# Performance work log

Hardware: AMD Instinct MI355X
Metric: run time of the kernel (lower is better)

## Reference

```python
import jax, jax.numpy as jnp
import numpy as np

N_NODES = 100000
N_EDGES = 3200000
EPS = 1e-5
NEG_SLOPE = 0.1


def _glorot(key, fan_in, fan_out):
    lim = np.sqrt(6.0 / (fan_in + fan_out))
    return jax.random.uniform(key, (fan_in, fan_out), jnp.float32, -lim, lim)


def setup_inputs() -> dict:
    key = jax.random.key(0)
    ks = jax.random.split(key, 16)
    x = jax.random.normal(ks[0], (N_NODES, 3), jnp.float32)
    edge_index = jax.random.randint(ks[1], (2, N_EDGES), 0, N_NODES, jnp.int32)
    dims = [(3, 64), (64, 64), (64, 256), (256, 256), (256, 512), (512, 1)]
    inp = {"x": x, "edge_index": edge_index}
    for i, (fi, fo) in enumerate(dims):
        inp[f"W{i+1}"] = _glorot(ks[2 + i], fi, fo)
        inp[f"b{i+1}"] = jnp.zeros((fo,), jnp.float32)
    for i, fo in enumerate([64, 64, 256, 256, 512]):
        inp[f"g{i+1}"] = jnp.ones((fo,), jnp.float32)
        inp[f"bt{i+1}"] = jnp.zeros((fo,), jnp.float32)
    return inp


def _gcn_conv(h, W, b, src, dst, dis):
    # transform first (cheaper when out_dim <= in_dim is not guaranteed, but
    # avoids gathering raw features twice); then edge-normalized scatter-add.
    hw = h @ W                                   # [N, Fo]
    norm = dis[src] * dis[dst]                   # [E]
    agg = jax.ops.segment_sum(hw[src] * norm[:, None], dst, num_segments=N_NODES)
    agg = agg + (dis * dis)[:, None] * hw        # self-loop term (norm = dis_i^2)
    return agg + b


def _bn(h, g, bt):
    mu = jnp.mean(h, axis=0)
    var = jnp.mean((h - mu) ** 2, axis=0)        # biased var, as torch BN
    return (h - mu) * jax.lax.rsqrt(var + EPS) * g + bt


def _lrelu(h):
    return jnp.where(h > 0, h, NEG_SLOPE * h)


def reference(x, edge_index, W1, b1, W2, b2, W3, b3, W4, b4, W5, b5, W6, b6,
              g1, bt1, g2, bt2, g3, bt3, g4, bt4, g5, bt5):
    src, dst = edge_index[0], edge_index[1]
    # degree includes the added self-loop (+1), symmetric normalization
    deg = jax.ops.segment_sum(jnp.ones((N_EDGES,), x.dtype), dst,
                              num_segments=N_NODES) + 1.0
    dis = jax.lax.rsqrt(deg)

    h = x
    Ws = [W1, W2, W3, W4, W5]
    bs = [b1, b2, b3, b4, b5]
    gs = [g1, g2, g3, g4, g5]
    bts = [bt1, bt2, bt3, bt4, bt5]
    for W, b, g, bt in zip(Ws, bs, gs, bts):
        h = _gcn_conv(h, W, b, src, dst, dis)
        h = _lrelu(_bn(h, g, bt))
    h = _gcn_conv(h, W6, b6, src, dst, dis)
    return jax.nn.sigmoid(h)
```

## Files before the change

kernel.cpp:

```cpp
#include <hip/hip_runtime.h>
#include <math.h>

typedef unsigned short u16;
typedef unsigned int u32;
typedef __attribute__((ext_vector_type(8))) short bf16x8;
typedef __attribute__((ext_vector_type(4))) float f32x4;
typedef __attribute__((ext_vector_type(2))) float f32x2;

constexpr float EPS_BN = 1e-5f;
constexpr float NEG = 0.1f;
constexpr int LDP = 800;

static inline int cdiv(int a, int b) { return (a + b - 1) / b; }


__device__ __forceinline__ float b2f_lo(u32 v) { return __uint_as_float(v << 16); }
__device__ __forceinline__ float b2f_hi(u32 v) { return __uint_as_float(v & 0xFFFF0000u); }
__device__ __forceinline__ float b2f(u16 v) { return __uint_as_float(((u32)v) << 16); }
__device__ __forceinline__ u16 f2b(float f) {
  u32 u = __float_as_uint(f);
  u32 r = u + 0x7FFFu + ((u >> 16) & 1u);
  return (u16)(r >> 16);
}
__device__ __forceinline__ u32 pack2(float a, float b) {
  return (u32)f2b(a) | ((u32)f2b(b) << 16);
}
__device__ __forceinline__ void unpack8(uint4 v, float* o) {
  o[0] = b2f_lo(v.x); o[1] = b2f_hi(v.x);
  o[2] = b2f_lo(v.y); o[3] = b2f_hi(v.y);
  o[4] = b2f_lo(v.z); o[5] = b2f_hi(v.z);
  o[6] = b2f_lo(v.w); o[7] = b2f_hi(v.w);
}

__device__ __forceinline__ void gload16(const void* g, void* l) {
  __builtin_amdgcn_global_load_lds(
      (const __attribute__((address_space(1))) u32*)g,
      (__attribute__((address_space(3))) u32*)l, 16, 0, 0);
}

__device__ __forceinline__ void bn8_acc(uint4 v, const f32x2* sc2, const f32x2* sh2,
                                        float d, f32x2* acc) {
  const f32x2 dd = {d, d};
  const f32x2 c01 = {NEG, NEG};
  const u32* w = &v.x;
#pragma unroll
  for (int p = 0; p < 4; ++p) {
    f32x2 z = {b2f_lo(w[p]), b2f_hi(w[p])};
    f32x2 t = z * sc2[p] + sh2[p];
    f32x2 q = __builtin_elementwise_max(t, t * c01);
    acc[p] = dd * q + acc[p];
  }
}


__global__ void k_zero_i32(int* p, int n) {
  int i = blockIdx.x * blockDim.x + threadIdx.x;
  if (i < n) p[i] = 0;
}

__global__ __launch_bounds__(256) void k_bcount(const int* __restrict__ dst,
                                                int* __restrict__ bucketCnt, int E) {
  __shared__ int hist[256];
  int tid = threadIdx.x;
  hist[tid] = 0;
  __syncthreads();
  int e0 = blockIdx.x * 4096;
#pragma unroll
  for (int i = 0; i < 16; ++i) {
    int e = e0 + i * 256 + tid;
    if (e < E) atomicAdd(&hist[dst[e] >> 9], 1);
  }
  __syncthreads();
  int h = hist[tid];
  if (h > 0) atomicAdd(&bucketCnt[tid], h);
}

__global__ void k_bscan(const int* __restrict__ bucketCnt, int* __restrict__ bucketOff,
                        int* __restrict__ bucketCur, int NB, int E) {
  __shared__ int s[256];
  int tid = threadIdx.x;
  int v = (tid < NB) ? bucketCnt[tid] : 0;
  s[tid] = v;
  __syncthreads();
  for (int off = 1; off < 256; off <<= 1) {
    int t = (tid >= off) ? s[tid - off] : 0;
    __syncthreads();
    s[tid] += t;
    __syncthreads();
  }
  if (tid < NB) bucketOff[tid] = s[tid] - v;
  if (tid == NB) bucketOff[NB] = E;
  if (tid < NB) bucketCur[tid] = 0;
}

__global__ __launch_bounds__(256) void k_bucket(const int* __restrict__ src,
                                                const int* __restrict__ dst,
                                                const int* __restrict__ bucketOff,
                                                int* __restrict__ bucketCur,
                                                u32* __restrict__ ebuf, int E) {
  __shared__ int hist[256];
  __shared__ int base[256];
  __shared__ int lcur[256];
  int tid = threadIdx.x;
  hist[tid] = 0; lcur[tid] = 0;
  __syncthreads();
  int e0 = blockIdx.x * 4096;
  int ss[16], dd[16];
#pragma unroll
  for (int i = 0; i < 16; ++i) {
    int e = e0 + i * 256 + tid;
    if (e < E) {
      ss[i] = src[e]; dd[i] = dst[e];
      atomicAdd(&hist[dd[i] >> 9], 1);
    } else dd[i] = -1;
  }
  __syncthreads();
  int h = hist[tid];
  if (h > 0) base[tid] = bucketOff[tid] + atomicAdd(&bucketCur[tid], h);
  __syncthreads();
#pragma unroll
  for (int i = 0; i < 16; ++i) {
    if (dd[i] >= 0) {
      int bk = dd[i] >> 9;
      int p = atomicAdd(&lcur[bk], 1);
      ebuf[base[bk] + p] = ((u32)ss[i] << 9) | ((u32)dd[i] & 511u);
    }
  }
}

__global__ __launch_bounds__(256) void k_csr(const u32* __restrict__ ebuf,
                                             const int* __restrict__ bucketOff,
                                             int* __restrict__ rowoff,
                                             int* __restrict__ col,
                                             float* __restrict__ dis,
                                             int N, int E, int NB) {
  __shared__ int hist[512];
  __shared__ int loff[512];
  __shared__ int scan_s[256];
  int b = blockIdx.x;
  int tid = threadIdx.x;
  int ebase = bucketOff[b], eend = bucketOff[b + 1];
  int ecnt = eend - ebase;
  hist[tid] = 0; hist[tid + 256] = 0;
  __syncthreads();
  for (int i = tid; i < ecnt; i += 256)
    atomicAdd(&hist[ebuf[ebase + i] & 511u], 1);
  __syncthreads();
  int h0 = hist[2 * tid], h1 = hist[2 * tid + 1];
  int ts = h0 + h1;
  scan_s[tid] = ts;
  __syncthreads();
  for (int off = 1; off < 256; off <<= 1) {
    int t = (tid >= off) ? scan_s[tid - off] : 0;
    __syncthreads();
    scan_s[tid] += t;
    __syncthreads();
  }
  int excl = scan_s[tid] - ts;
  loff[2 * tid] = excl;
  loff[2 * tid + 1] = excl + h0;
  __syncthreads();
  int gbase = b * 512;
  for (int i = tid; i < 512; i += 256) {
    int node = gbase + i;
    if (node < N) {
      rowoff[node] = ebase + loff[i];
      dis[node] = rsqrtf((float)hist[i] + 1.0f);
    }
  }
  if (b == NB - 1 && tid == 0) rowoff[N] = E;
  __syncthreads();
  for (int i = tid; i < ecnt; i += 256) {
    u32 ed = ebuf[ebase + i];
    int p = atomicAdd(&loff[ed & 511u], 1);
    col[ebase + p] = (int)(ed >> 9);
  }
}


__global__ void k_xd(const float* __restrict__ x, const float* __restrict__ dis,
                     float4* __restrict__ xd, int n) {
  int i = blockIdx.x * blockDim.x + threadIdx.x;
  if (i >= n) return;
  float d = dis[i];
  xd[i] = make_float4(d * x[i * 3 + 0], d * x[i * 3 + 1], d * x[i * 3 + 2], 0.f);
}

__global__ void k_l1(const float4* __restrict__ xd, const int* __restrict__ rowoff,
                     const int* __restrict__ col, const float* __restrict__ dis,
                     const float* __restrict__ W, const float* __restrict__ b,
                     u16* __restrict__ z, int n) {
  int wid = (blockIdx.x * blockDim.x + threadIdx.x) >> 6;
  int lane = threadIdx.x & 63;
  if (wid >= n) return;
  float a0 = 0.f, a1 = 0.f, a2 = 0.f;
  int beg = rowoff[wid], end = rowoff[wid + 1];
  for (int e = beg + lane; e < end; e += 64) {
    float4 v = xd[col[e]];
    a0 += v.x; a1 += v.y; a2 += v.z;
  }
#pragma unroll
  for (int off = 32; off; off >>= 1) {
    a0 += __shfl_xor(a0, off); a1 += __shfl_xor(a1, off); a2 += __shfl_xor(a2, off);
  }
  float di = dis[wid];
  float4 sv = xd[wid];
  a0 = di * (a0 + sv.x);
  a1 = di * (a1 + sv.y);
  a2 = di * (a2 + sv.z);
  float zv = a0 * W[lane] + a1 * W[64 + lane] + a2 * W[128 + lane] + b[lane];
  z[(size_t)wid * 64 + lane] = f2b(zv);
}


__global__ void k_agg64(const u16* __restrict__ z, const int* __restrict__ rowoff,
                        const int* __restrict__ col, const float* __restrict__ dis,
                        const float* __restrict__ scaleF, const float* __restrict__ shiftF,
                        u16* __restrict__ a, int n) {
  int wid = (blockIdx.x * blockDim.x + threadIdx.x) >> 6;
  int lane = threadIdx.x & 63;
  if (wid >= n) return;
  int sub = lane >> 3, c = lane & 7;
  const uint4* z4 = (const uint4*)z;
  f32x2 sc2[4], sh2[4];
#pragma unroll
  for (int p = 0; p < 4; ++p) {
    sc2[p] = *(const f32x2*)&scaleF[c * 8 + p * 2];
    sh2[p] = *(const f32x2*)&shiftF[c * 8 + p * 2];
  }
  f32x2 acc[4] = {{0.f, 0.f}, {0.f, 0.f}, {0.f, 0.f}, {0.f, 0.f}};
  int beg = rowoff[wid], end = rowoff[wid + 1];
  int e = beg + sub;
  int j1 = (e < end) ? col[e] : -1;
  int j2 = (e + 8 < end) ? col[e + 8] : -1;
  float d1 = (j1 >= 0) ? dis[j1] : 0.f;
  float d2 = (j2 >= 0) ? dis[j2] : 0.f;
  while (j1 >= 0) {
    int en = e + 16;
    int nj1 = -1, nj2 = -1;
    if (j2 >= 0) {
      if (en < end) nj1 = col[en];
      if (en + 8 < end) nj2 = col[en + 8];
    }
    float nd1 = (nj1 >= 0) ? dis[nj1] : 0.f;
    float nd2 = (nj2 >= 0) ? dis[nj2] : 0.f;
    bn8_acc(z4[(size_t)j1 * 8 + c], sc2, sh2, d1, acc);
    if (j2 >= 0) bn8_acc(z4[(size_t)j2 * 8 + c], sc2, sh2, d2, acc);
    e = en; j1 = nj1; j2 = nj2; d1 = nd1; d2 = nd2;
  }
  float* af = (float*)acc;
#pragma unroll
  for (int k = 0; k < 8; ++k) {
    af[k] += __shfl_xor(af[k], 8);
    af[k] += __shfl_xor(af[k], 16);
    af[k] += __shfl_xor(af[k], 32);
  }
  if (sub == 0) {
    float dw = dis[wid];
    bn8_acc(z4[(size_t)wid * 8 + c], sc2, sh2, dw, acc);
    uint4 r;
    r.x = pack2(dw * af[0], dw * af[1]);
    r.y = pack2(dw * af[2], dw * af[3]);
    r.z = pack2(dw * af[4], dw * af[5]);
    r.w = pack2(dw * af[6], dw * af[7]);
    ((uint4*)a)[(size_t)wid * 8 + c] = r;
  }
}

__global__ void k_agg256(const u16* __restrict__ z, const int* __restrict__ rowoff,
                         const int* __restrict__ col, const float* __restrict__ dis,
                         const float* __restrict__ scaleF, const float* __restrict__ shiftF,
                         u16* __restrict__ a, int n) {
  int wid = (blockIdx.x * blockDim.x + threadIdx.x) >> 6;
  int lane = threadIdx.x & 63;
  if (wid >= n) return;
  int sub = lane >> 5, c = lane & 31;
  const uint4* z4 = (const uint4*)z;
  f32x2 sc2[4], sh2[4];
#pragma unroll
  for (int p = 0; p < 4; ++p) {
    sc2[p] = *(const f32x2*)&scaleF[c * 8 + p * 2];
    sh2[p] = *(const f32x2*)&shiftF[c * 8 + p * 2];
  }
  f32x2 acc[4] = {{0.f, 0.f}, {0.f, 0.f}, {0.f, 0.f}, {0.f, 0.f}};
  int beg = rowoff[wid], end = rowoff[wid + 1];
  int e = beg + sub;
  int j1 = (e < end) ? col[e] : -1;
  int j2 = (e + 2 < end) ? col[e + 2] : -1;
  float d1 = (j1 >= 0) ? dis[j1] : 0.f;
  float d2 = (j2 >= 0) ? dis[j2] : 0.f;
  while (j1 >= 0) {
    int en = e + 4;
    int nj1 = -1, nj2 = -1;
    if (j2 >= 0) {
      if (en < end) nj1 = col[en];
      if (en + 2 < end) nj2 = col[en + 2];
    }
    float nd1 = (nj1 >= 0) ? dis[nj1] : 0.f;
    float nd2 = (nj2 >= 0) ? dis[nj2] : 0.f;
    bn8_acc(z4[(size_t)j1 * 32 + c], sc2, sh2, d1, acc);
    if (j2 >= 0) bn8_acc(z4[(size_t)j2 * 32 + c], sc2, sh2, d2, acc);
    e = en; j1 = nj1; j2 = nj2; d1 = nd1; d2 = nd2;
  }
  float* af = (float*)acc;
#pragma unroll
  for (int k = 0; k < 8; ++k) af[k] += __shfl_xor(af[k], 32);
  if (sub == 0) {
    float dw = dis[wid];
    bn8_acc(z4[(size_t)wid * 32 + c], sc2, sh2, dw, acc);
    uint4 r;
    r.x = pack2(dw * af[0], dw * af[1]);
    r.y = pack2(dw * af[2], dw * af[3]);
    r.z = pack2(dw * af[4], dw * af[5]);
    r.w = pack2(dw * af[6], dw * af[7]);
    ((uint4*)a)[(size_t)wid * 32 + c] = r;
  }
}


__global__ void k_wt_all(const float* __restrict__ W2, const float* __restrict__ W3,
                         const float* __restrict__ W4, const float* __restrict__ W5,
                         u16* __restrict__ WT) {
  int i = blockIdx.x * blockDim.x + threadIdx.x;
  const float* W; int K, Fo, base;
  if (i < 4096)        { W = W2; K = 64;  Fo = 64;  base = 0; }
  else if (i < 20480)  { W = W3; K = 64;  Fo = 256; base = 4096; }
  else if (i < 86016)  { W = W4; K = 256; Fo = 256; base = 20480; }
  else if (i < 217088) { W = W5; K = 256; Fo = 512; base = 86016; }
  else return;
  int idx = i - base;
  int f = idx / K, k = idx - f * K;
  WT[i] = f2b(W[(size_t)k * Fo + f]);
}


__global__ __launch_bounds__(256) void k_gemm(const u16* __restrict__ A,
                                              const u16* __restrict__ WT,
                                              const float* __restrict__ bias,
                                              u16* __restrict__ C,
                                              float* __restrict__ psum,
                                              float* __restrict__ psq,
                                              int n, int K, int Fo, int nby) {
  __shared__ u16 As[128 * 64];
  __shared__ u16 Bs[128 * 64];
  int tid = threadIdx.x;
  int nwg = gridDim.x;
  int bid = blockIdx.x;
  int q = nwg >> 3, rr = nwg & 7;
  int xcd = bid & 7, pos = bid >> 3;
  int wgid = (xcd < rr ? xcd * (q + 1) : rr * (q + 1) + (xcd - rr) * q) + pos;
  int bx = wgid / nby, by = wgid - bx * nby;
  int bm0 = bx * 128, bn0 = by * 128;
  int lane = tid & 63, wv = tid >> 6;
  int wm = wv >> 1, wn = wv & 1;
  int fr = lane & 15, fg = lane >> 4;
  int srow = lane >> 3;
  int cb = (lane & 7) ^ srow;
  f32x4 acc[4][4];
#pragma unroll
  for (int i = 0; i < 4; ++i)
#pragma unroll
    for (int j = 0; j < 4; ++j) acc[i][j] = (f32x4)0.0f;

  for (int kt = 0; kt < K; kt += 64) {
#pragma unroll
    for (int i = 0; i < 4; ++i) {
      int rb = 8 * (4 * wv + i);
      const u16* ga = &A[(size_t)(bm0 + rb + srow) * K + kt + cb * 8];
      gload16(ga, &As[rb * 64 + lane * 8]);
      const u16* gb = &WT[(size_t)(bn0 + rb + srow) * K + kt + cb * 8];
      gload16(gb, &Bs[rb * 64 + lane * 8]);
    }
    __syncthreads();
#pragma unroll
    for (int ks = 0; ks < 2; ++ks) {
      int k0 = ks * 32 + fg * 8;
      bf16x8 af[4], bf[4];
#pragma unroll
      for (int mi = 0; mi < 4; ++mi) {
        int row = wm * 64 + mi * 16 + fr;
        int byt = (row * 128 + k0 * 2) ^ ((row & 7) << 4);
        af[mi] = *(const bf16x8*)((const char*)As + byt);
      }
#pragma unroll
      for (int ni = 0; ni < 4; ++ni) {
        int row = wn * 64 + ni * 16 + fr;
        int byt = (row * 128 + k0 * 2) ^ ((row & 7) << 4);
        bf[ni] = *(const bf16x8*)((const char*)Bs + byt);
      }
#pragma unroll
      for (int mi = 0; mi < 4; ++mi)
#pragma unroll
        for (int ni = 0; ni < 4; ++ni)
          acc[mi][ni] = __builtin_amdgcn_mfma_f32_16x16x32_bf16(af[mi], bf[ni], acc[mi][ni], 0, 0, 0);
    }
    __syncthreads();
  }
  float* s2 = (float*)&As[0];
#pragma unroll
  for (int ni = 0; ni < 4; ++ni) {
    int gc = bn0 + wn * 64 + ni * 16 + fr;
    float ps = 0.f, pq = 0.f;
    if (gc < Fo) {
      float bv = bias[gc];
#pragma unroll
      for (int mi = 0; mi < 4; ++mi) {
#pragma unroll
        for (int rg = 0; rg < 4; ++rg) {
          int gr = bm0 + wm * 64 + mi * 16 + fg * 4 + rg;
          if (gr < n) {
            float v = acc[mi][ni][rg] + bv;
            C[(size_t)gr * Fo + gc] = f2b(v);
            ps += v; pq += v * v;
          }
        }
      }
    }
    ps += __shfl_xor(ps, 16); ps += __shfl_xor(ps, 32);
    pq += __shfl_xor(pq, 16); pq += __shfl_xor(pq, 32);
    if (fg == 0 && gc < Fo) {
      int cl = wn * 64 + ni * 16 + fr;
      s2[wm * 128 + cl] = ps;
      s2[256 + wm * 128 + cl] = pq;
    }
  }
  __syncthreads();
  if (tid < 128) {
    int gc = bn0 + tid;
    if (gc < Fo) {
      psum[(size_t)gc * LDP + bx] = s2[tid] + s2[128 + tid];
      psq[(size_t)gc * LDP + bx] = s2[256 + tid] + s2[384 + tid];
    }
  }
}


__global__ void k_colred(const u16* __restrict__ z, int Fo, int n, int rowsPerChunk,
                         float* __restrict__ psum, float* __restrict__ psq) {
  int fl = threadIdx.x & 63;
  int rg = threadIdx.x >> 6;
  int f = blockIdx.y * 64 + fl;
  int r0 = blockIdx.x * rowsPerChunk;
  int r1 = min(n, r0 + rowsPerChunk);
  float s = 0.f, sq = 0.f;
  for (int r = r0 + rg; r < r1; r += 4) {
    float v = b2f(z[(size_t)r * Fo + f]);
    s += v;
    sq += v * v;
  }
  __shared__ float ls[4][64], lq[4][64];
  ls[rg][fl] = s; lq[rg][fl] = sq;
  __syncthreads();
  if (rg == 0) {
    psum[(size_t)f * LDP + blockIdx.x] = ls[0][fl] + ls[1][fl] + ls[2][fl] + ls[3][fl];
    psq[(size_t)f * LDP + blockIdx.x] = lq[0][fl] + lq[1][fl] + lq[2][fl] + lq[3][fl];
  }
}

__global__ void k_bnparams(const float* __restrict__ psum, const float* __restrict__ psq,
                           int Fo, int nChunks, int n,
                           const float* __restrict__ g, const float* __restrict__ bt,
                           float* __restrict__ scaleF, float* __restrict__ shiftF) {
  int f = blockIdx.x * 4 + (threadIdx.x >> 6);
  int lane = threadIdx.x & 63;
  if (f >= Fo) return;
  float s = 0.f, sq = 0.f;
  const float* ps = &psum[(size_t)f * LDP];
  const float* pq = &psq[(size_t)f * LDP];
  for (int c = lane; c < nChunks; c += 64) { s += ps[c]; sq += pq[c]; }
#pragma unroll
  for (int off = 32; off; off >>= 1) {
    s += __shfl_xor(s, off);
    sq += __shfl_xor(sq, off);
  }
  if (lane == 0) {
    float inv = 1.0f / (float)n;
    float mu = s * inv;
    float var = sq * inv - mu * mu;
    float rs = rsqrtf(var + EPS_BN) * g[f];
    scaleF[f] = rs;
    shiftF[f] = bt[f] - mu * rs;
  }
}


__global__ void k_dot512(const u16* __restrict__ z, const float* __restrict__ scaleF,
                         const float* __restrict__ shiftF, const float* __restrict__ w6,
                         const float* __restrict__ dis, float* __restrict__ v, int n) {
  __shared__ float ws[512], scs[512], shs[512];
  int tid = threadIdx.x;
  for (int i = tid; i < 512; i += 256) { ws[i] = w6[i]; scs[i] = scaleF[i]; shs[i] = shiftF[i]; }
  __syncthreads();
  int lane = tid % 64, wv = tid / 64;
  int node = blockIdx.x * 4 + wv;
  if (node >= n) return;
  uint4 vz = *(const uint4*)&z[(size_t)node * 512 + lane * 8];
  float f[8];
  unpack8(vz, f);
  int f0 = lane * 8;
  float s = 0.f;
#pragma unroll
  for (int k = 0; k < 8; ++k) {
    float a = f[k] * scs[f0 + k] + shs[f0 + k];
    a = (a > 0.f) ? a : NEG * a;
    s += a * ws[f0 + k];
  }
#pragma unroll
  for (int off = 32; off > 0; off >>= 1) s += __shfl_down(s, off);
  if (lane == 0) v[node] = dis[node] * s;
}

__global__ void k_final(const float* __restrict__ v, const int* __restrict__ rowoff,
                        const int* __restrict__ col, const float* __restrict__ dis,
                        const float* __restrict__ b6, float* __restrict__ out, int n) {
  int wid = (blockIdx.x * blockDim.x + threadIdx.x) >> 6;
  int lane = threadIdx.x & 63;
  if (wid >= n) return;
  float acc = 0.f;
  int beg = rowoff[wid], end = rowoff[wid + 1];
  for (int e = beg + lane; e < end; e += 64) acc += v[col[e]];
#pragma unroll
  for (int off = 32; off; off >>= 1) acc += __shfl_xor(acc, off);
  if (lane == 0) {
    float zz = dis[wid] * (acc + v[wid]) + b6[0];
    out[wid] = 1.0f / (1.0f + expf(-zz));
  }
}


extern "C" void kernel_launch(void* const* d_in, const int* in_sizes, int n_in,
                              void* d_out, int out_size, void* d_ws, size_t ws_size,
                              hipStream_t stream) {
  const float* x = (const float*)d_in[0];
  const int* ei = (const int*)d_in[1];
  const int N = in_sizes[0] / 3;
  const int E = in_sizes[1] / 2;
  const int* srcIdx = ei;
  const int* dstIdx = ei + E;

  const float* W[6]; const float* b[6];
  for (int i = 0; i < 6; ++i) { W[i] = (const float*)d_in[2 + 2 * i]; b[i] = (const float*)d_in[3 + 2 * i]; }
  const float* g[5]; const float* bt[5];
  for (int i = 0; i < 5; ++i) { g[i] = (const float*)d_in[14 + 2 * i]; bt[i] = (const float*)d_in[15 + 2 * i]; }

  char* wsB = (char*)d_ws;
  size_t off = 0;
  auto alloc = [&](size_t bytes) -> void* {
    void* p = wsB + off;
    off = (off + bytes + 255) & ~(size_t)255;
    return p;
  };

  const int NB = cdiv(N, 512);
  int* rowoff = (int*)alloc((size_t)(N + 1) * 4);
  int* col = (int*)alloc((size_t)E * 4);
  float* dis = (float*)alloc((size_t)N * 4);
  float* vbuf = (float*)alloc((size_t)N * 4);
  float* scaleF = (float*)alloc(512 * 4);
  float* shiftF = (float*)alloc(512 * 4);
  float4* xd = (float4*)alloc((size_t)N * 16);
  u16* WTb = (u16*)alloc((size_t)217088 * 2);
  int* bucketCnt = (int*)alloc(256 * 4);
  int* bucketOff = (int*)alloc(257 * 4);
  int* bucketCur = (int*)alloc(256 * 4);
  const int nbx = cdiv(N, 128);
  float* psum = (float*)alloc((size_t)512 * LDP * 4);
  float* psq = (float*)alloc((size_t)512 * LDP * 4);
  u16* Zb = (u16*)alloc((size_t)N * 512 * 2);
  u16* Ab = (u16*)alloc((size_t)(N + 128) * 256 * 2);
  u32* ebuf = (u32*)Ab;

  const int wtOff[5] = {0, 0, 4096, 20480, 86016};
  k_wt_all<<<cdiv(217088, 256), 256, 0, stream>>>(W[1], W[2], W[3], W[4], WTb);

  const int EB = cdiv(E, 4096);
  k_zero_i32<<<1, 256, 0, stream>>>(bucketCnt, 256);
  k_bcount<<<EB, 256, 0, stream>>>(dstIdx, bucketCnt, E);
  k_bscan<<<1, 256, 0, stream>>>(bucketCnt, bucketOff, bucketCur, NB, E);
  k_bucket<<<EB, 256, 0, stream>>>(srcIdx, dstIdx, bucketOff, bucketCur, ebuf, E);
  k_csr<<<NB, 256, 0, stream>>>(ebuf, bucketOff, rowoff, col, dis, N, E, NB);

  auto gemm = [&](const u16* Ain, int layer, int K, int Fo, u16* Cout) {
    int nby = cdiv(Fo, 128);
    k_gemm<<<nbx * nby, 256, 0, stream>>>(Ain, WTb + wtOff[layer], b[layer], Cout,
                                          psum, psq, N, K, Fo, nby);
    k_bnparams<<<cdiv(Fo, 4), 256, 0, stream>>>(psum, psq, Fo, nbx, N,
                                                g[layer], bt[layer], scaleF, shiftF);
  };

  const int waveGrid = cdiv(N * 64, 256);

  k_xd<<<cdiv(N, 256), 256, 0, stream>>>(x, dis, xd, N);
  k_l1<<<waveGrid, 256, 0, stream>>>(xd, rowoff, col, dis, W[0], b[0], Zb, N);
  {
    const int rowsPerChunk = 2048;
    const int nChunks = cdiv(N, rowsPerChunk);
    dim3 grid(nChunks, 1);
    k_colred<<<grid, 256, 0, stream>>>(Zb, 64, N, rowsPerChunk, psum, psq);
    k_bnparams<<<cdiv(64, 4), 256, 0, stream>>>(psum, psq, 64, nChunks, N, g[0], bt[0], scaleF, shiftF);
  }

  k_agg64<<<waveGrid, 256, 0, stream>>>(Zb, rowoff, col, dis, scaleF, shiftF, Ab, N);
  gemm(Ab, 1, 64, 64, Zb);

  k_agg64<<<waveGrid, 256, 0, stream>>>(Zb, rowoff, col, dis, scaleF, shiftF, Ab, N);
  gemm(Ab, 2, 64, 256, Zb);

  k_agg256<<<waveGrid, 256, 0, stream>>>(Zb, rowoff, col, dis, scaleF, shiftF, Ab, N);
  gemm(Ab, 3, 256, 256, Zb);

  k_agg256<<<waveGrid, 256, 0, stream>>>(Zb, rowoff, col, dis, scaleF, shiftF, Ab, N);
  gemm(Ab, 4, 256, 512, Zb);

  k_dot512<<<cdiv(N, 4), 256, 0, stream>>>(Zb, scaleF, shiftF, W[5], dis, vbuf, N);
  k_final<<<waveGrid, 256, 0, stream>>>(vbuf, rowoff, col, dis, b[5], (float*)d_out, N);
}
```

Measured before the change: 1.154 ms.

## Split aggregation feature columns across XCD halves and fold xd into CSR build

```diff
diff --git a/kernel.cpp b/kernel.cpp
--- a/kernel.cpp
+++ b/kernel.cpp
@@ -130,9 +130,11 @@
 
 __global__ __launch_bounds__(256) void k_csr(const u32* __restrict__ ebuf,
                                              const int* __restrict__ bucketOff,
+                                             const float* __restrict__ x,
                                              int* __restrict__ rowoff,
                                              int* __restrict__ col,
                                              float* __restrict__ dis,
+                                             float4* __restrict__ xd,
                                              int N, int E, int NB) {
   __shared__ int hist[512];
   __shared__ int loff[512];
@@ -165,7 +167,10 @@
     int node = gbase + i;
     if (node < N) {
       rowoff[node] = ebase + loff[i];
-      dis[node] = rsqrtf((float)hist[i] + 1.0f);
+      float d = rsqrtf((float)hist[i] + 1.0f);
+      dis[node] = d;
+      xd[node] = make_float4(d * x[node * 3 + 0], d * x[node * 3 + 1],
+                             d * x[node * 3 + 2], 0.f);
     }
   }
   if (b == NB - 1 && tid == 0) rowoff[N] = E;
@@ -177,14 +182,6 @@
   }
 }
 
-
-__global__ void k_xd(const float* __restrict__ x, const float* __restrict__ dis,
-                     float4* __restrict__ xd, int n) {
-  int i = blockIdx.x * blockDim.x + threadIdx.x;
-  if (i >= n) return;
-  float d = dis[i];
-  xd[i] = make_float4(d * x[i * 3 + 0], d * x[i * 3 + 1], d * x[i * 3 + 2], 0.f);
-}
 
 __global__ void k_l1(const float4* __restrict__ xd, const int* __restrict__ rowoff,
                      const int* __restrict__ col, const float* __restrict__ dis,
@@ -217,53 +214,60 @@
                         const int* __restrict__ col, const float* __restrict__ dis,
                         const float* __restrict__ scaleF, const float* __restrict__ shiftF,
                         u16* __restrict__ a, int n) {
-  int wid = (blockIdx.x * blockDim.x + threadIdx.x) >> 6;
+  int bid = blockIdx.x;
+  int xcd = bid & 7;
+  int half = xcd >> 2;
+  int slot = ((bid >> 3) << 2) + (xcd & 3);
+  int node = (slot << 2) + (threadIdx.x >> 6);
+  if (node >= n) return;
   int lane = threadIdx.x & 63;
-  if (wid >= n) return;
-  int sub = lane >> 3, c = lane & 7;
+  int sub = lane >> 2, c = lane & 3;
   const uint4* z4 = (const uint4*)z;
   f32x2 sc2[4], sh2[4];
+  int f0 = half * 32 + c * 8;
 #pragma unroll
   for (int p = 0; p < 4; ++p) {
-    sc2[p] = *(const f32x2*)&scaleF[c * 8 + p * 2];
-    sh2[p] = *(const f32x2*)&shiftF[c * 8 + p * 2];
-  }
+    sc2[p] = *(const f32x2*)&scaleF[f0 + p * 2];
+    sh2[p] = *(const f32x2*)&shiftF[f0 + p * 2];
+  }
+  int rb = half * 4 + c;
   f32x2 acc[4] = {{0.f, 0.f}, {0.f, 0.f}, {0.f, 0.f}, {0.f, 0.f}};
-  int beg = rowoff[wid], end = rowoff[wid + 1];
+  int beg = rowoff[node], end = rowoff[node + 1];
   int e = beg + sub;
   int j1 = (e < end) ? col[e] : -1;
-  int j2 = (e + 8 < end) ? col[e + 8] : -1;
+  int j2 = (e + 16 < end) ? col[e + 16] : -1;
   float d1 = (j1 >= 0) ? dis[j1] : 0.f;
   float d2 = (j2 >= 0) ? dis[j2] : 0.f;
   while (j1 >= 0) {
-    int en = e + 16;
+    int en = e + 32;
     int nj1 = -1, nj2 = -1;
     if (j2 >= 0) {
       if (en < end) nj1 = col[en];
-      if (en + 8 < end) nj2 = col[en + 8];
+      if (en + 16 < end) nj2 = col[en + 16];
     }
     float nd1 = (nj1 >= 0) ? dis[nj1] : 0.f;
     float nd2 = (nj2 >= 0) ? dis[nj2] : 0.f;
-    bn8_acc(z4[(size_t)j1 * 8 + c], sc2, sh2, d1, acc);
-    if (j2 >= 0) bn8_acc(z4[(size_t)j2 * 8 + c], sc2, sh2, d2, acc);
+    bn8_acc(z4[(size_t)j1 * 8 + rb], sc2, sh2, d1, acc);
+    if (j2 >= 0) bn8_acc(z4[(size_t)j2 * 8 + rb], sc2, sh2, d2, acc);
     e = en; j1 = nj1; j2 = nj2; d1 = nd1; d2 = nd2;
   }
   float* af = (float*)acc;
 #pragma unroll
   for (int k = 0; k < 8; ++k) {
+    af[k] += __shfl_xor(af[k], 4);
     af[k] += __shfl_xor(af[k], 8);
     af[k] += __shfl_xor(af[k], 16);
     af[k] += __shfl_xor(af[k], 32);
   }
   if (sub == 0) {
-    float dw = dis[wid];
-    bn8_acc(z4[(size_t)wid * 8 + c], sc2, sh2, dw, acc);
+    float dw = dis[node];
+    bn8_acc(z4[(size_t)node * 8 + rb], sc2, sh2, dw, acc);
     uint4 r;
     r.x = pack2(dw * af[0], dw * af[1]);
     r.y = pack2(dw * af[2], dw * af[3]);
     r.z = pack2(dw * af[4], dw * af[5]);
     r.w = pack2(dw * af[6], dw * af[7]);
-    ((uint4*)a)[(size_t)wid * 8 + c] = r;
+    ((uint4*)a)[(size_t)node * 8 + rb] = r;
   }
 }
 
@@ -271,49 +275,58 @@
                          const int* __restrict__ col, const float* __restrict__ dis,
                          const float* __restrict__ scaleF, const float* __restrict__ shiftF,
                          u16* __restrict__ a, int n) {
-  int wid = (blockIdx.x * blockDim.x + threadIdx.x) >> 6;
+  int bid = blockIdx.x;
+  int xcd = bid & 7;
+  int half = xcd >> 2;
+  int slot = ((bid >> 3) << 2) + (xcd & 3);
+  int node = (slot << 2) + (threadIdx.x >> 6);
+  if (node >= n) return;
   int lane = threadIdx.x & 63;
-  if (wid >= n) return;
-  int sub = lane >> 5, c = lane & 31;
+  int sub = lane >> 4, c = lane & 15;
   const uint4* z4 = (const uint4*)z;
   f32x2 sc2[4], sh2[4];
+  int f0 = half * 128 + c * 8;
 #pragma unroll
   for (int p = 0; p < 4; ++p) {
-    sc2[p] = *(const f32x2*)&scaleF[c * 8 + p * 2];
-    sh2[p] = *(const f32x2*)&shiftF[c * 8 + p * 2];
-  }
+    sc2[p] = *(const f32x2*)&scaleF[f0 + p * 2];
+    sh2[p] = *(const f32x2*)&shiftF[f0 + p * 2];
+  }
+  int rb = half * 16 + c;
   f32x2 acc[4] = {{0.f, 0.f}, {0.f, 0.f}, {0.f, 0.f}, {0.f, 0.f}};
-  int beg = rowoff[wid], end = rowoff[wid + 1];
+  int beg = rowoff[node], end = rowoff[node + 1];
   int e = beg + sub;
   int j1 = (e < end) ? col[e] : -1;
-  int j2 = (e + 2 < end) ? col[e + 2] : -1;
+  int j2 = (e + 4 < end) ? col[e + 4] : -1;
   float d1 = (j1 >= 0) ? dis[j1] : 0.f;
   float d2 = (j2 >= 0) ? dis[j2] : 0.f;
   while (j1 >= 0) {
-    int en = e + 4;
+    int en = e + 8;
     int nj1 = -1, nj2 = -1;
     if (j2 >= 0) {
       if (en < end) nj1 = col[en];
-      if (en + 2 < end) nj2 = col[en + 2];
+      if (en + 4 < end) nj2 = col[en + 4];
     }
     float nd1 = (nj1 >= 0) ? dis[nj1] : 0.f;
     float nd2 = (nj2 >= 0) ? dis[nj2] : 0.f;
-    bn8_acc(z4[(size_t)j1 * 32 + c], sc2, sh2, d1, acc);
-    if (j2 >= 0) bn8_acc(z4[(size_t)j2 * 32 + c], sc2, sh2, d2, acc);
+    bn8_acc(z4[(size_t)j1 * 32 + rb], sc2, sh2, d1, acc);
+    if (j2 >= 0) bn8_acc(z4[(size_t)j2 * 32 + rb], sc2, sh2, d2, acc);
     e = en; j1 = nj1; j2 = nj2; d1 = nd1; d2 = nd2;
   }
   float* af = (float*)acc;
 #pragma unroll
-  for (int k = 0; k < 8; ++k) af[k] += __shfl_xor(af[k], 32);
+  for (int k = 0; k < 8; ++k) {
+    af[k] += __shfl_xor(af[k], 16);
+    af[k] += __shfl_xor(af[k], 32);
+  }
   if (sub == 0) {
-    float dw = dis[wid];
-    bn8_acc(z4[(size_t)wid * 32 + c], sc2, sh2, dw, acc);
+    float dw = dis[node];
+    bn8_acc(z4[(size_t)node * 32 + rb], sc2, sh2, dw, acc);
     uint4 r;
     r.x = pack2(dw * af[0], dw * af[1]);
     r.y = pack2(dw * af[2], dw * af[3]);
     r.z = pack2(dw * af[4], dw * af[5]);
     r.w = pack2(dw * af[6], dw * af[7]);
-    ((uint4*)a)[(size_t)wid * 32 + c] = r;
+    ((uint4*)a)[(size_t)node * 32 + rb] = r;
   }
 }
 
@@ -578,7 +591,7 @@
   k_bcount<<<EB, 256, 0, stream>>>(dstIdx, bucketCnt, E);
   k_bscan<<<1, 256, 0, stream>>>(bucketCnt, bucketOff, bucketCur, NB, E);
   k_bucket<<<EB, 256, 0, stream>>>(srcIdx, dstIdx, bucketOff, bucketCur, ebuf, E);
-  k_csr<<<NB, 256, 0, stream>>>(ebuf, bucketOff, rowoff, col, dis, N, E, NB);
+  k_csr<<<NB, 256, 0, stream>>>(ebuf, bucketOff, x, rowoff, col, dis, xd, N, E, NB);
 
   auto gemm = [&](const u16* Ain, int layer, int K, int Fo, u16* Cout) {
     int nby = cdiv(Fo, 128);
@@ -589,8 +602,8 @@
   };
 
   const int waveGrid = cdiv(N * 64, 256);
-
-  k_xd<<<cdiv(N, 256), 256, 0, stream>>>(x, dis, xd, N);
+  const int aggGrid = 8 * cdiv(cdiv(N, 4), 4);
+
   k_l1<<<waveGrid, 256, 0, stream>>>(xd, rowoff, col, dis, W[0], b[0], Zb, N);
   {
     const int rowsPerChunk = 2048;
@@ -600,16 +613,16 @@
     k_bnparams<<<cdiv(64, 4), 256, 0, stream>>>(psum, psq, 64, nChunks, N, g[0], bt[0], scaleF, shiftF);
   }
 
-  k_agg64<<<waveGrid, 256, 0, stream>>>(Zb, rowoff, col, dis, scaleF, shiftF, Ab, N);
+  k_agg64<<<aggGrid, 256, 0, stream>>>(Zb, rowoff, col, dis, scaleF, shiftF, Ab, N);
   gemm(Ab, 1, 64, 64, Zb);
 
-  k_agg64<<<waveGrid, 256, 0, stream>>>(Zb, rowoff, col, dis, scaleF, shiftF, Ab, N);
+  k_agg64<<<aggGrid, 256, 0, stream>>>(Zb, rowoff, col, dis, scaleF, shiftF, Ab, N);
   gemm(Ab, 2, 64, 256, Zb);
 
-  k_agg256<<<waveGrid, 256, 0, stream>>>(Zb, rowoff, col, dis, scaleF, shiftF, Ab, N);
+  k_agg256<<<aggGrid, 256, 0, stream>>>(Zb, rowoff, col, dis, scaleF, shiftF, Ab, N);
   gemm(Ab, 3, 256, 256, Zb);
 
-  k_agg256<<<waveGrid, 256, 0, stream>>>(Zb, rowoff, col, dis, scaleF, shiftF, Ab, N);
+  k_agg256<<<aggGrid, 256, 0, stream>>>(Zb, rowoff, col, dis, scaleF, shiftF, Ab, N);
   gemm(Ab, 4, 256, 512, Zb);
 
   k_dot512<<<cdiv(N, 4), 256, 0, stream>>>(Zb, scaleF, shiftF, W[5], dis, vbuf, N);
```

New measurement: 1.224 ms. +6.0%, slower.
